# Optimization experiments

Hardware: AMD Instinct MI355X
Metric: run time of the kernel (lower is better)

## Reference

```python
import jax, jax.numpy as jnp
import numpy as np

EPS = 1e-5

def bn(x, gamma, beta, axes):
    # Training-mode batch norm: normalize over batch(+spatial) axes, channel-last layout.
    m = x.mean(axes, keepdims=True)
    v = x.var(axes, keepdims=True)
    return gamma * (x - m) * jax.lax.rsqrt(v + EPS) + beta

def spa_group(k, xyz, feat):
    # PCT-style grouping: k-NN in xyz space, concat(neighbor-center, center).
    # xyz: (B,N,3)  feat: (B,N,C)  ->  (B,N,k,2C)
    sq = jnp.sum(xyz * xyz, axis=-1)  # (B,N)
    d = sq[:, :, None] + sq[:, None, :] - 2.0 * jnp.einsum('bnd,bmd->bnm', xyz, xyz)
    _, idx = jax.lax.top_k(-d, k)  # (B,N,k) nearest-neighbor indices (includes self)
    grouped = jax.vmap(lambda f, i: f[i])(feat, idx)  # (B,N,k,C) irregular gather
    center = feat[:, :, None, :]
    return jnp.concatenate([grouped - center, jnp.broadcast_to(center, grouped.shape)], axis=-1)

def local_op(x, w1, g1, b1, w2, g2, b2):
    # x: (B,N,K,Ci) -> conv1x1/BN/ReLU x2 over the K window, then max-pool over K -> (B,N,Co)
    h = jnp.einsum('bnkc,oc->bnko', x, w1)
    h = jax.nn.relu(bn(h, g1, b1, (0, 1, 2)))
    h = jnp.einsum('bnkc,oc->bnko', h, w2)
    h = jax.nn.relu(bn(h, g2, b2, (0, 1, 2)))
    return h.max(axis=2)

def setup_inputs():
    key = jax.random.key(0)
    ks = jax.random.split(key, 7)
    B, N = 4, 2048
    d_i, d_h1, d_h2, d_h3, d_o = 3, 64, 256, 512, 1024
    def w(k_, o, i):
        return jax.random.normal(k_, (o, i), jnp.float32) * (1.0 / np.sqrt(i))
    return {
        'xyz': jax.random.normal(ks[0], (B, N, d_i), jnp.float32),
        'w_c1': w(ks[1], d_h1, d_i), 'g_c1': jnp.ones((d_h1,), jnp.float32), 'b_c1': jnp.zeros((d_h1,), jnp.float32),
        'w_c2': w(ks[2], d_h2, d_h1), 'g_c2': jnp.ones((d_h2,), jnp.float32), 'b_c2': jnp.zeros((d_h2,), jnp.float32),
        'w_l0a': w(ks[3], d_h3, d_h3), 'g_l0a': jnp.ones((d_h3,), jnp.float32), 'b_l0a': jnp.zeros((d_h3,), jnp.float32),
        'w_l0b': w(ks[4], d_h3, d_h3), 'g_l0b': jnp.ones((d_h3,), jnp.float32), 'b_l0b': jnp.zeros((d_h3,), jnp.float32),
        'w_l1a': w(ks[5], d_o, d_o), 'g_l1a': jnp.ones((d_o,), jnp.float32), 'b_l1a': jnp.zeros((d_o,), jnp.float32),
        'w_l1b': w(ks[6], d_o, d_o), 'g_l1b': jnp.ones((d_o,), jnp.float32), 'b_l1b': jnp.zeros((d_o,), jnp.float32),
        'k': 8,
    }

def reference(xyz, w_c1, g_c1, b_c1, w_c2, g_c2, b_c2,
              w_l0a, g_l0a, b_l0a, w_l0b, g_l0b, b_l0b,
              w_l1a, g_l1a, b_l1a, w_l1b, g_l1b, b_l1b, k):
    # Stem: conv1x1-BN-ReLU x2 in (B,N,C) layout (equivalent to torch (B,C,N) with BN over (0,2))
    h = jax.nn.relu(bn(jnp.einsum('bnc,oc->bno', xyz, w_c1), g_c1, b_c1, (0, 1)))
    h = jax.nn.relu(bn(jnp.einsum('bnc,oc->bno', h, w_c2), g_c2, b_c2, (0, 1)))
    g = spa_group(k, xyz, h)                                   # (B,N,k,512)
    h = local_op(g, w_l0a, g_l0a, b_l0a, w_l0b, g_l0b, b_l0b)  # (B,N,512)
    g = spa_group(k, xyz, h)                                   # (B,N,k,1024)
    h = local_op(g, w_l1a, g_l1a, b_l1a, w_l1b, g_l1b, b_l1b)  # (B,N,1024)
    return jnp.transpose(h, (0, 2, 1))  # (B, d_o, N) to match torch output layout
```

## Files before the change

### kernel.cpp

```cpp
#include <hip/hip_runtime.h>

typedef unsigned short u16;
typedef __attribute__((ext_vector_type(8))) short s16x8;
typedef __attribute__((ext_vector_type(8))) __bf16 bf16x8;
typedef __attribute__((ext_vector_type(8))) unsigned short u16x8;
typedef __attribute__((ext_vector_type(4))) float f32x4;

#define BN_EPS 1e-5f

__device__ u16   g_Z[(size_t)65536 * 1024];
__device__ u16   g_F[(size_t)8192 * 2048];
__device__ float g_pooled[(size_t)8192 * 1024];
__device__ float g_h2pre[8192 * 256];
__device__ u16   g_h2b[8192 * 256];
__device__ u16   g_hl0b[8192 * 512];
__device__ float g_y1[8192 * 64];
__device__ u16   g_wm0a[1024 * 256];
__device__ u16   g_w0b[512 * 512];
__device__ u16   g_wm1a[2048 * 512];
__device__ u16   g_w1b[1024 * 1024];
__device__ int   g_nidx[65536];
__device__ float g_st[24 * 1024];

#define S(i) (g_st + (i) * 1024)

static __device__ __forceinline__ float bf2f(u16 u) {
  unsigned int x = ((unsigned int)u) << 16;
  return __builtin_bit_cast(float, x);
}
static __device__ __forceinline__ u16 f2bf(float f) {
  unsigned int x = __builtin_bit_cast(unsigned int, f);
  x += 0x7fffu + ((x >> 16) & 1u);
  return (u16)(x >> 16);
}
static __device__ __forceinline__ f32x4 mfma16x16(s16x8 a, s16x8 b, f32x4 c) {
  return __builtin_amdgcn_mfma_f32_16x16x32_bf16(
      __builtin_bit_cast(bf16x8, a), __builtin_bit_cast(bf16x8, b), c, 0, 0, 0);
}
static __device__ __forceinline__ void gl_lds16(const void* g, void* l) {
  __builtin_amdgcn_global_load_lds((const __attribute__((address_space(1))) void*)g,
                                   (__attribute__((address_space(3))) void*)l, 16, 0, 0);
}

__global__ void k_zero() {
  int i = blockIdx.x * 256 + threadIdx.x;
  if (i < 12 * 1024) g_st[i] = 0.f;
}

__global__ void k_lin1(const float* __restrict__ xyz, const float* __restrict__ w) {
  __shared__ float ls[64], lq[64];
  int t = threadIdx.x;
  if (t < 64) { ls[t] = 0.f; lq[t] = 0.f; }
  __syncthreads();
  int e = blockIdx.x * 256 + t;
  int row = e >> 6, ch = e & 63;
  float x0 = xyz[row * 3], x1 = xyz[row * 3 + 1], x2 = xyz[row * 3 + 2];
  float v = x0 * w[ch * 3] + x1 * w[ch * 3 + 1] + x2 * w[ch * 3 + 2];
  g_y1[e] = v;
  atomicAdd(&ls[ch], v);
  atomicAdd(&lq[ch], v * v);
  __syncthreads();
  if (t < 64) { atomicAdd(&S(0)[t], ls[t]); atomicAdd(&S(1)[t], lq[t]); }
}

__global__ void k_stats(const float* __restrict__ g, const float* __restrict__ b,
                        int si_s, int si_q, int si_sc, int si_bi, float invcnt) {
  int c = blockIdx.x * 64 + threadIdx.x;
  float m = S(si_s)[c] * invcnt;
  float v = S(si_q)[c] * invcnt - m * m;
  float sc = g[c] * rsqrtf(v + BN_EPS);
  S(si_sc)[c] = sc;
  S(si_bi)[c] = b[c] - m * sc;
}

__global__ void k_lin2(const float* __restrict__ w) {
  __shared__ float hrow[64];
  int t = threadIdx.x;
  float wr[64];
#pragma unroll
  for (int i = 0; i < 64; i++) wr[i] = w[t * 64 + i];
  const float* sc1 = S(12);
  const float* bi1 = S(13);
  float ps = 0.f, pq = 0.f;
  int r0 = blockIdx.x * 16;
  for (int r = 0; r < 16; r++) {
    if (t < 64) {
      float v = g_y1[(r0 + r) * 64 + t];
      v = v * sc1[t] + bi1[t];
      hrow[t] = v > 0.f ? v : 0.f;
    }
    __syncthreads();
    float acc = 0.f;
#pragma unroll
    for (int i = 0; i < 64; i++) acc += hrow[i] * wr[i];
    g_h2pre[(r0 + r) * 256 + t] = acc;
    ps += acc;
    pq += acc * acc;
    __syncthreads();
  }
  atomicAdd(&S(2)[t], ps);
  atomicAdd(&S(3)[t], pq);
}

__global__ void k_bnrelu_h2() {
  int i = blockIdx.x * 256 + threadIdx.x;
  if (i >= 8192 * 256) return;
  int c = i & 255;
  float v = g_h2pre[i] * S(14)[c] + S(15)[c];
  g_h2b[i] = f2bf(v > 0.f ? v : 0.f);
}

__global__ __launch_bounds__(256) void k_knn(const float* __restrict__ xyz) {
  int t = threadIdx.x, lane = t & 63, w = t >> 6;
  int qn = blockIdx.x * 4 + w;
  int b = qn >> 11;
  const float* xb = xyz + (size_t)b * 2048 * 3;
  int ql = qn & 2047;
  float qx = xb[ql * 3], qy = xb[ql * 3 + 1], qz = xb[ql * 3 + 2];
  float qsq = qx * qx + qy * qy + qz * qz;

  float bd[8];
  int bi[8];
#pragma unroll
  for (int i = 0; i < 8; i++) { bd[i] = 1e30f; bi[i] = 0x7fffffff; }

#pragma unroll 4
  for (int i = 0; i < 32; i++) {
    int j = lane + i * 64;
    float x = xb[j * 3], y = xb[j * 3 + 1], z = xb[j * 3 + 2];
    float sq = x * x + y * y + z * z;
    float d = qsq + sq - 2.0f * (qx * x + qy * y + qz * z);
    if (d < bd[7]) {
      bd[7] = d; bi[7] = j;
#pragma unroll
      for (int p = 7; p > 0; p--) {
        if (bd[p] < bd[p - 1]) {
          float td = bd[p]; bd[p] = bd[p - 1]; bd[p - 1] = td;
          int ti = bi[p]; bi[p] = bi[p - 1]; bi[p - 1] = ti;
        }
      }
    }
  }

  int keep = 0;
#pragma unroll
  for (int r = 0; r < 8; r++) {
    float md = bd[0];
    int mi = bi[0];
#pragma unroll
    for (int s = 1; s < 64; s <<= 1) {
      float od = __shfl_xor(md, s, 64);
      int oi = __shfl_xor(mi, s, 64);
      if (od < md || (od == md && oi < mi)) { md = od; mi = oi; }
    }
    bool own = (bd[0] == md) && (bi[0] == mi);
    if (own) {
#pragma unroll
      for (int p = 0; p < 7; p++) { bd[p] = bd[p + 1]; bi[p] = bi[p + 1]; }
      bd[7] = 1e30f; bi[7] = 0x7fffffff;
    }
    if (lane == r) keep = mi;
  }
  if (lane < 8) g_nidx[qn * 8 + lane] = b * 2048 + keep;
}

__global__ void k_prep_w(const float* __restrict__ src, int which, int n) {
  int i = blockIdx.x * 256 + threadIdx.x;
  if (i >= n) return;
  u16* dst = which == 1 ? g_w0b : g_w1b;
  dst[i] = f2bf(src[i]);
}

__global__ void k_prep_wst(const float* __restrict__ src, int which, int lc, int N, int n) {
  int i = blockIdx.x * 256 + threadIdx.x;
  if (i >= n) return;
  int C = 1 << lc;
  int r = i >> lc, c = i & (C - 1);
  float v;
  if (r < N) v = src[r * 2 * C + c];
  else { int o = r - N; v = src[o * 2 * C + C + c] - src[o * 2 * C + c]; }
  u16* dst = which == 0 ? g_wm0a : g_wm1a;
  dst[i] = f2bf(v);
}


#define GEMM_PRO()                                                     \
  int t = threadIdx.x, lane = t & 63, w = t >> 6;                      \
  int chunk = gridDim.x >> 3;                                          \
  int idx = ((int)blockIdx.x & 7) * chunk + ((int)blockIdx.x >> 3);    \
  int bx = idx & ((1 << lbx) - 1), by = idx >> lbx;                    \
  int wm = w >> 2, wn = w & 3;                                         \
  int l15 = lane & 15, lq = lane >> 4;                                 \
  int gcs = (((lane & 3) ^ ((lane >> 3) & 3))) * 8;                    \
  int rA0 = w * 16 + (lane >> 2), rA1 = rA0 + 128;                     \
  int ldsA0 = w * 512, ldsA1 = 4096 + w * 512;                         \
  int ksw = (lq ^ ((l15 >> 1) & 3)) * 8;                               \
  f32x4 acc[8][4];                                                     \
  _Pragma("unroll") for (int m = 0; m < 8; m++)                        \
  _Pragma("unroll") for (int n = 0; n < 4; n++)                        \
      acc[m][n] = f32x4{0.f, 0.f, 0.f, 0.f};

#define GEMM_LOOP(STG)                                                   \
  STG(0, 0) STG(1, 1) STG(2, 2)                                          \
  asm volatile("s_waitcnt vmcnt(8)" ::: "memory");                       \
  __builtin_amdgcn_s_barrier();                                          \
  asm volatile("" ::: "memory");                                         \
  for (int ks = 0; ks < nk; ks++) {                                      \
    int b = ks & 3;                                                      \
    int kst = (ks + 3 < nk) ? ks + 3 : nk - 1;                           \
    STG(kst, (ks + 3) & 3)                                               \
    s16x8 af[8], bf[4];                                                  \
    _Pragma("unroll") for (int m = 0; m < 8; m++)                        \
        af[m] = *(const s16x8*)&As[b][(wm * 128 + m * 16 + l15) * 32 + ksw]; \
    _Pragma("unroll") for (int n = 0; n < 4; n++)                        \
        bf[n] = *(const s16x8*)&Bs[b][(wn * 64 + n * 16 + l15) * 32 + ksw];  \
    __builtin_amdgcn_s_setprio(1);                                       \
    _Pragma("unroll") for (int m = 0; m < 8; m++)                        \
    _Pragma("unroll") for (int n = 0; n < 4; n++)                        \
        acc[m][n] = mfma16x16(af[m], bf[n], acc[m][n]);                  \
    __builtin_amdgcn_s_setprio(0);                                       \
    asm volatile("s_waitcnt vmcnt(8)" ::: "memory");                     \
    __builtin_amdgcn_s_barrier();                                        \
    asm volatile("" ::: "memory");                                       \
  }

#define GEMM_STATS(si_s, si_q)                                           \
  if (t < 256) { cs[t] = 0.f; cq[t] = 0.f; }                             \
  __syncthreads();                                                       \
  _Pragma("unroll") for (int n = 0; n < 4; n++) {                        \
    float ssum = 0.f, ssq = 0.f;                                         \
    _Pragma("unroll") for (int m = 0; m < 8; m++)                        \
    _Pragma("unroll") for (int j = 0; j < 4; j++) {                      \
      float v = acc[m][n][j];                                            \
      ssum += v;                                                         \
      ssq += v * v;                                                      \
    }                                                                    \
    int col = wn * 64 + n * 16 + l15;                                    \
    atomicAdd(&cs[col], ssum);                                           \
    atomicAdd(&cq[col], ssq);                                            \
  }                                                                      \
  __syncthreads();                                                       \
  if (t < 256) {                                                         \
    atomicAdd(&S(si_s)[bx * 256 + t], cs[t]);                            \
    atomicAdd(&S(si_q)[bx * 256 + t], cq[t]);                            \
  }

__global__ __launch_bounds__(512) void k_fgemm(int layer, int C, int N2, int lbx) {
  __shared__ u16 As[4][8192];
  __shared__ u16 Bs[4][8192];
  const u16* feat = layer == 0 ? g_h2b : g_hl0b;
  const u16* W = layer == 0 ? g_wm0a : g_wm1a;
  GEMM_PRO();
  int nk = C >> 5;
  const u16* srA0 = feat + (size_t)(by * 256 + rA0) * C + gcs;
  const u16* srA1 = feat + (size_t)(by * 256 + rA1) * C + gcs;
  const u16* srB0 = W + (size_t)(bx * 256 + rA0) * C + gcs;
  const u16* srB1 = W + (size_t)(bx * 256 + rA1) * C + gcs;

#define STG_F(KT, BUF)                                                        \
  {                                                                           \
    int kg_ = (KT) * 32;                                                      \
    gl_lds16(srA0 + kg_, &As[BUF][ldsA0]);                                    \
    gl_lds16(srA1 + kg_, &As[BUF][ldsA1]);                                    \
    gl_lds16(srB0 + kg_, &Bs[BUF][ldsA0]);                                    \
    gl_lds16(srB1 + kg_, &Bs[BUF][ldsA1]);                                    \
  }

  GEMM_LOOP(STG_F)
#undef STG_F

#pragma unroll
  for (int m = 0; m < 8; m++) {
    int rbase = by * 256 + wm * 128 + m * 16 + lq * 4;
#pragma unroll
    for (int n = 0; n < 4; n++) {
      int col = bx * 256 + wn * 64 + n * 16 + l15;
#pragma unroll
      for (int j = 0; j < 4; j++)
        g_F[(size_t)(rbase + j) * N2 + col] = f2bf(acc[m][n][j]);
    }
  }
}

__global__ __launch_bounds__(512) void k_combine(int N, int lgc, int si_s, int si_q) {
  __shared__ float Ls[1024], Lq[1024];
  int t = threadIdx.x;
  int chs8 = 1 << lgc;
  int c8 = t & (chs8 - 1);
  int g = t >> lgc;
  int G = 512 >> lgc;
  int rpg = 256 / G;
  int row0 = blockIdx.x * 256 + g * rpg;
  int ch0 = c8 * 8;
  int N2 = 2 * N;
  float ss[8], sq[8];
#pragma unroll
  for (int j = 0; j < 8; j++) { ss[j] = 0.f; sq[j] = 0.f; }

  for (int r = row0; r < row0 + rpg; r++) {
    int nb = g_nidx[r];
    int ct = r >> 3;
    u16x8 a = *(const u16x8*)(g_F + (size_t)nb * N2 + ch0);
    u16x8 b = *(const u16x8*)(g_F + (size_t)ct * N2 + N + ch0);
    u16x8 o;
#pragma unroll
    for (int j = 0; j < 8; j++) {
      float z = bf2f(a[j]) + bf2f(b[j]);
      o[j] = f2bf(z);
      ss[j] += z;
      sq[j] += z * z;
    }
    *(u16x8*)(g_Z + (size_t)r * N + ch0) = o;
  }

  for (int c = t; c < N; c += 512) { Ls[c] = 0.f; Lq[c] = 0.f; }
  __syncthreads();
#pragma unroll
  for (int j = 0; j < 8; j++) {
    atomicAdd(&Ls[ch0 + j], ss[j]);
    atomicAdd(&Lq[ch0 + j], sq[j]);
  }
  __syncthreads();
  for (int c = t; c < N; c += 512) {
    atomicAdd(&S(si_s)[c], Ls[c]);
    atomicAdd(&S(si_q)[c], Lq[c]);
  }
}

__global__ __launch_bounds__(512) void k_gp8(int layer, int K, int N, int si_s,
                                             int si_q, int lbx) {
  __shared__ u16 As[4][8192];
  __shared__ u16 Bs[4][8192];
  __shared__ float cs[256], cq[256];
  const u16* W = layer == 0 ? g_w0b : g_w1b;
  GEMM_PRO();
  int nk = K >> 5;
  const u16* srA0 = g_Z + (size_t)(by * 256 + rA0) * K + gcs;
  const u16* srA1 = g_Z + (size_t)(by * 256 + rA1) * K + gcs;
  const u16* srB0 = W + (size_t)(bx * 256 + rA0) * K + gcs;
  const u16* srB1 = W + (size_t)(bx * 256 + rA1) * K + gcs;

#define STG_P(KT, BUF)                                                        \
  {                                                                           \
    int kg_ = (KT) * 32;                                                      \
    gl_lds16(srA0 + kg_, &As[BUF][ldsA0]);                                    \
    gl_lds16(srA1 + kg_, &As[BUF][ldsA1]);                                    \
    gl_lds16(srB0 + kg_, &Bs[BUF][ldsA0]);                                    \
    gl_lds16(srB1 + kg_, &Bs[BUF][ldsA1]);                                    \
  }

  GEMM_LOOP(STG_P)
#undef STG_P

#pragma unroll
  for (int m = 0; m < 8; m++) {
    int prow = by * 32 + wm * 16 + m * 2 + (lq >> 1);
#pragma unroll
    for (int n = 0; n < 4; n++) {
      float v4 = fmaxf(fmaxf(acc[m][n][0], acc[m][n][1]), fmaxf(acc[m][n][2], acc[m][n][3]));
      float v8 = fmaxf(v4, __shfl_xor(v4, 16, 64));
      if ((lane & 16) == 0) {
        int col = bx * 256 + wn * 64 + n * 16 + l15;
        g_pooled[(size_t)prow * N + col] = v8;
      }
    }
  }
  GEMM_STATS(si_s, si_q)
}

__global__ void k_bnrelu_z(int si_sc, int si_bi, int cmask, size_t n8) {
  size_t i = (size_t)blockIdx.x * 256 + threadIdx.x;
  size_t stride = (size_t)gridDim.x * 256;
  const float* sc = S(si_sc);
  const float* bi = S(si_bi);
  for (; i < n8; i += stride) {
    u16x8 v = *(const u16x8*)(g_Z + i * 8);
    int c0 = (int)((i * 8) & (size_t)cmask);
    u16x8 o;
#pragma unroll
    for (int j = 0; j < 8; j++) {
      float f = bf2f(v[j]) * sc[c0 + j] + bi[c0 + j];
      o[j] = f2bf(f > 0.f ? f : 0.f);
    }
    *(u16x8*)(g_Z + i * 8) = o;
  }
}

__global__ void k_bnrelu_pool() {
  int i = blockIdx.x * 256 + threadIdx.x;
  if (i >= 8192 * 512) return;
  int c = i & 511;
  float v = g_pooled[i] * S(18)[c] + S(19)[c];
  g_hl0b[i] = f2bf(v > 0.f ? v : 0.f);
}

__global__ void k_final_t(float* __restrict__ out) {
  __shared__ float tile[64][65];
  int b = blockIdx.z;
  int nb = blockIdx.y;
  int cb = blockIdx.x;
  int t = threadIdx.x;
  int cl = t & 63;
  int c = cb * 64 + cl;
  float sc = S(22)[c], bi = S(23)[c];
  for (int nl = t >> 6; nl < 64; nl += 4) {
    float v = g_pooled[(size_t)(b * 2048 + nb * 64 + nl) * 1024 + c] * sc + bi;
    tile[nl][cl] = v > 0.f ? v : 0.f;
  }
  __syncthreads();
  int nl2 = t & 63;
  for (int ci = t >> 6; ci < 64; ci += 4) {
    out[((size_t)b * 1024 + cb * 64 + ci) * 2048 + nb * 64 + nl2] = tile[nl2][ci];
  }
}

extern "C" void kernel_launch(void* const* d_in, const int* in_sizes, int n_in,
                              void* d_out, int out_size, void* d_ws, size_t ws_size,
                              hipStream_t stream) {
  const float* xyz  = (const float*)d_in[0];
  const float* w_c1 = (const float*)d_in[1];
  const float* g_c1 = (const float*)d_in[2];
  const float* b_c1 = (const float*)d_in[3];
  const float* w_c2 = (const float*)d_in[4];
  const float* g_c2 = (const float*)d_in[5];
  const float* b_c2 = (const float*)d_in[6];
  const float* w_l0a = (const float*)d_in[7];
  const float* g_l0a = (const float*)d_in[8];
  const float* b_l0a = (const float*)d_in[9];
  const float* w_l0b = (const float*)d_in[10];
  const float* g_l0b = (const float*)d_in[11];
  const float* b_l0b = (const float*)d_in[12];
  const float* w_l1a = (const float*)d_in[13];
  const float* g_l1a = (const float*)d_in[14];
  const float* b_l1a = (const float*)d_in[15];
  const float* w_l1b = (const float*)d_in[16];
  const float* g_l1b = (const float*)d_in[17];
  const float* b_l1b = (const float*)d_in[18];
  float* out = (float*)d_out;

  k_zero<<<48, 256, 0, stream>>>();

  k_lin1<<<2048, 256, 0, stream>>>(xyz, w_c1);
  k_stats<<<1, 64, 0, stream>>>(g_c1, b_c1, 0, 1, 12, 13, 1.f / 8192.f);
  k_lin2<<<512, 256, 0, stream>>>(w_c2);
  k_stats<<<4, 64, 0, stream>>>(g_c2, b_c2, 2, 3, 14, 15, 1.f / 8192.f);
  k_bnrelu_h2<<<8192, 256, 0, stream>>>();

  k_knn<<<2048, 256, 0, stream>>>(xyz);

  k_prep_wst<<<1024, 256, 0, stream>>>(w_l0a, 0, 8, 512, 262144);
  k_prep_w<<<1024, 256, 0, stream>>>(w_l0b, 1, 262144);
  k_prep_wst<<<4096, 256, 0, stream>>>(w_l1a, 2, 9, 1024, 1048576);
  k_prep_w<<<4096, 256, 0, stream>>>(w_l1b, 3, 1048576);

  k_fgemm<<<128, 512, 0, stream>>>(0, 256, 1024, 2);
  k_combine<<<256, 512, 0, stream>>>(512, 6, 4, 5);
  k_stats<<<8, 64, 0, stream>>>(g_l0a, b_l0a, 4, 5, 16, 17, 1.f / 65536.f);
  k_bnrelu_z<<<2048, 256, 0, stream>>>(16, 17, 511, (size_t)65536 * 512 / 8);
  k_gp8<<<512, 512, 0, stream>>>(0, 512, 512, 6, 7, 1);
  k_stats<<<8, 64, 0, stream>>>(g_l0b, b_l0b, 6, 7, 18, 19, 1.f / 65536.f);
  k_bnrelu_pool<<<16384, 256, 0, stream>>>();

  k_fgemm<<<256, 512, 0, stream>>>(1, 512, 2048, 3);
  k_combine<<<256, 512, 0, stream>>>(1024, 7, 8, 9);
  k_stats<<<16, 64, 0, stream>>>(g_l1a, b_l1a, 8, 9, 20, 21, 1.f / 65536.f);
  k_bnrelu_z<<<2048, 256, 0, stream>>>(20, 21, 1023, (size_t)65536 * 1024 / 8);
  k_gp8<<<1024, 512, 0, stream>>>(1, 1024, 1024, 10, 11, 2);
  k_stats<<<16, 64, 0, stream>>>(g_l1b, b_l1b, 10, 11, 22, 23, 1.f / 65536.f);
  k_final_t<<<dim3(16, 32, 4), 256, 0, stream>>>(out);
}
```

Measured before the change: 773.4 us.

## Restructure GEMM mainloop into 8-wave ping-pong with BK=64 double buffering

Replaces the 4-stage BK=32 LDS ring in both GEMM kernels with a double-buffered BK=64 tile and a new XOR swizzle. Each k-tile is split into four quadrant MFMA phases, with barriers between them, and the global-to-LDS loads for tile k+2 are interleaved between phases. The goal is to overlap LDS reads, global prefetch and MFMA work more finely and to cut per-k-step barrier overhead. The cost is more barriers per tile, tighter vmcnt bookkeeping, and only two buffers of prefetch depth.

```diff
diff --git a/kernel.cpp b/kernel.cpp
--- a/kernel.cpp
+++ b/kernel.cpp
@@ -184,44 +184,118 @@
 }
 
 
-#define GEMM_PRO()                                                     \
-  int t = threadIdx.x, lane = t & 63, w = t >> 6;                      \
-  int chunk = gridDim.x >> 3;                                          \
-  int idx = ((int)blockIdx.x & 7) * chunk + ((int)blockIdx.x >> 3);    \
-  int bx = idx & ((1 << lbx) - 1), by = idx >> lbx;                    \
-  int wm = w >> 2, wn = w & 3;                                         \
-  int l15 = lane & 15, lq = lane >> 4;                                 \
-  int gcs = (((lane & 3) ^ ((lane >> 3) & 3))) * 8;                    \
-  int rA0 = w * 16 + (lane >> 2), rA1 = rA0 + 128;                     \
-  int ldsA0 = w * 512, ldsA1 = 4096 + w * 512;                         \
-  int ksw = (lq ^ ((l15 >> 1) & 3)) * 8;                               \
-  f32x4 acc[8][4];                                                     \
-  _Pragma("unroll") for (int m = 0; m < 8; m++)                        \
-  _Pragma("unroll") for (int n = 0; n < 4; n++)                        \
+#define BARRIER_F() { __builtin_amdgcn_s_barrier(); asm volatile("" ::: "memory"); }
+
+#define GEMM8_PRO()                                                       \
+  int t = threadIdx.x, lane = t & 63, w = t >> 6;                         \
+  int chunk = gridDim.x >> 3;                                             \
+  int idx = ((int)blockIdx.x & 7) * chunk + ((int)blockIdx.x >> 3);       \
+  int bx = idx & ((1 << lbx) - 1), by = idx >> lbx;                       \
+  int wm = w >> 2, wn = w & 3;                                            \
+  int l15 = lane & 15, lq = lane >> 4;                                    \
+  int c0 = lq ^ (l15 & 7);                                                \
+  int ab0 = wm * 8192 + l15 * 64 + c0 * 8;                                \
+  int ab1 = wm * 8192 + l15 * 64 + (c0 ^ 4) * 8;                          \
+  int bb0 = (wn >> 1) * 8192 + (wn & 1) * 4096 + l15 * 64 + c0 * 8;       \
+  int bb1 = (wn >> 1) * 8192 + (wn & 1) * 4096 + l15 * 64 + (c0 ^ 4) * 8; \
+  int sr = t >> 3, skc = (t & 7) ^ ((t >> 3) & 7);                        \
+  f32x4 acc[8][4];                                                        \
+  _Pragma("unroll") for (int m = 0; m < 8; m++)                           \
+  _Pragma("unroll") for (int n = 0; n < 4; n++)                           \
       acc[m][n] = f32x4{0.f, 0.f, 0.f, 0.f};
 
-#define GEMM_LOOP(STG)                                                   \
-  STG(0, 0) STG(1, 1) STG(2, 2)                                          \
-  asm volatile("s_waitcnt vmcnt(8)" ::: "memory");                       \
-  __builtin_amdgcn_s_barrier();                                          \
-  asm volatile("" ::: "memory");                                         \
-  for (int ks = 0; ks < nk; ks++) {                                      \
-    int b = ks & 3;                                                      \
-    int kst = (ks + 3 < nk) ? ks + 3 : nk - 1;                           \
-    STG(kst, (ks + 3) & 3)                                               \
-    s16x8 af[8], bf[4];                                                  \
-    _Pragma("unroll") for (int m = 0; m < 8; m++)                        \
-        af[m] = *(const s16x8*)&As[b][(wm * 128 + m * 16 + l15) * 32 + ksw]; \
-    _Pragma("unroll") for (int n = 0; n < 4; n++)                        \
-        bf[n] = *(const s16x8*)&Bs[b][(wn * 64 + n * 16 + l15) * 32 + ksw];  \
-    __builtin_amdgcn_s_setprio(1);                                       \
-    _Pragma("unroll") for (int m = 0; m < 8; m++)                        \
-    _Pragma("unroll") for (int n = 0; n < 4; n++)                        \
-        acc[m][n] = mfma16x16(af[m], bf[n], acc[m][n]);                  \
-    __builtin_amdgcn_s_setprio(0);                                       \
-    asm volatile("s_waitcnt vmcnt(8)" ::: "memory");                     \
-    __builtin_amdgcn_s_barrier();                                        \
-    asm volatile("" ::: "memory");                                       \
+#define GEMM8_LOOP(Ag, Bg)                                                    \
+  const u16* a0 = (Ag) + (size_t)(by * 256 + sr) * K + skc * 8;               \
+  const u16* b0 = (Bg) + (size_t)(bx * 256 + sr) * K + skc * 8;               \
+  _Pragma("unroll") for (int tl = 0; tl < 2; tl++) {                          \
+    u16* AW = As + tl * 16384; u16* BW = Bs + tl * 16384;                     \
+    int cc = tl * 64;                                                         \
+    gl_lds16(a0 + cc, AW + t * 8);                                            \
+    gl_lds16(a0 + (size_t)128 * K + cc, AW + 8192 + t * 8);                   \
+    gl_lds16(a0 + (size_t)64 * K + cc, AW + 4096 + t * 8);                    \
+    gl_lds16(a0 + (size_t)192 * K + cc, AW + 12288 + t * 8);                  \
+    gl_lds16(b0 + cc, BW + t * 8);                                            \
+    gl_lds16(b0 + (size_t)64 * K + cc, BW + 4096 + t * 8);                    \
+    gl_lds16(b0 + (size_t)128 * K + cc, BW + 8192 + t * 8);                   \
+    gl_lds16(b0 + (size_t)192 * K + cc, BW + 12288 + t * 8);                  \
+  }                                                                           \
+  asm volatile("s_waitcnt vmcnt(8)" ::: "memory");                            \
+  BARRIER_F();                                                                \
+  for (int kt = 0; kt < nk; kt++) {                                           \
+    u16* AsR = As + (kt & 1) * 16384;                                         \
+    u16* BsR = Bs + (kt & 1) * 16384;                                         \
+    bool st = (kt + 2 < nk);                                                  \
+    int c2 = (kt + 2) * 64;                                                   \
+    s16x8 af[8], bfl[4], bfh[4];                                              \
+                                       \
+    _Pragma("unroll") for (int ks = 0; ks < 2; ks++)                          \
+    _Pragma("unroll") for (int m = 0; m < 4; m++)                             \
+        af[ks * 4 + m] = *(const s16x8*)&AsR[(ks ? ab1 : ab0) + m * 1024];    \
+    _Pragma("unroll") for (int ks = 0; ks < 2; ks++)                          \
+    _Pragma("unroll") for (int n = 0; n < 2; n++)                             \
+        bfl[ks * 2 + n] = *(const s16x8*)&BsR[(ks ? bb1 : bb0) + n * 1024];   \
+    BARRIER_F();                                                              \
+    asm volatile("s_waitcnt lgkmcnt(0)" ::: "memory");                        \
+    __builtin_amdgcn_sched_barrier(0);                                        \
+    __builtin_amdgcn_s_setprio(1);                                            \
+    _Pragma("unroll") for (int ks = 0; ks < 2; ks++)                          \
+    _Pragma("unroll") for (int m = 0; m < 4; m++)                             \
+    _Pragma("unroll") for (int n = 0; n < 2; n++)                             \
+        acc[m][n] = mfma16x16(af[ks * 4 + m], bfl[ks * 2 + n], acc[m][n]);    \
+    __builtin_amdgcn_s_setprio(0);                                            \
+    BARRIER_F();                                                              \
+       \
+    if (st) {                                                                 \
+      gl_lds16(a0 + c2, AsR + t * 8);                                         \
+      gl_lds16(a0 + (size_t)128 * K + c2, AsR + 8192 + t * 8);                \
+    }                                                                         \
+    _Pragma("unroll") for (int ks = 0; ks < 2; ks++)                          \
+    _Pragma("unroll") for (int n = 0; n < 2; n++)                             \
+        bfh[ks * 2 + n] = *(const s16x8*)&BsR[(ks ? bb1 : bb0) + 2048 + n * 1024]; \
+    BARRIER_F();                                                              \
+    asm volatile("s_waitcnt lgkmcnt(0)" ::: "memory");                        \
+    __builtin_amdgcn_sched_barrier(0);                                        \
+    __builtin_amdgcn_s_setprio(1);                                            \
+    _Pragma("unroll") for (int ks = 0; ks < 2; ks++)                          \
+    _Pragma("unroll") for (int m = 0; m < 4; m++)                             \
+    _Pragma("unroll") for (int n = 0; n < 2; n++)                             \
+        acc[m][2 + n] = mfma16x16(af[ks * 4 + m], bfh[ks * 2 + n], acc[m][2 + n]); \
+    __builtin_amdgcn_s_setprio(0);                                            \
+    BARRIER_F();                                                              \
+                      \
+    if (st) {                                                                 \
+      gl_lds16(b0 + c2, BsR + t * 8);                                         \
+      gl_lds16(b0 + (size_t)64 * K + c2, BsR + 4096 + t * 8);                 \
+      gl_lds16(b0 + (size_t)128 * K + c2, BsR + 8192 + t * 8);                \
+      gl_lds16(b0 + (size_t)192 * K + c2, BsR + 12288 + t * 8);               \
+    }                                                                         \
+    _Pragma("unroll") for (int ks = 0; ks < 2; ks++)                          \
+    _Pragma("unroll") for (int m = 0; m < 4; m++)                             \
+        af[ks * 4 + m] = *(const s16x8*)&AsR[(ks ? ab1 : ab0) + 4096 + m * 1024]; \
+    BARRIER_F();                                                              \
+    asm volatile("s_waitcnt lgkmcnt(0)" ::: "memory");                        \
+    __builtin_amdgcn_sched_barrier(0);                                        \
+    __builtin_amdgcn_s_setprio(1);                                            \
+    _Pragma("unroll") for (int ks = 0; ks < 2; ks++)                          \
+    _Pragma("unroll") for (int m = 0; m < 4; m++)                             \
+    _Pragma("unroll") for (int n = 0; n < 2; n++)                             \
+        acc[4 + m][n] = mfma16x16(af[ks * 4 + m], bfl[ks * 2 + n], acc[4 + m][n]); \
+    __builtin_amdgcn_s_setprio(0);                                            \
+    BARRIER_F();                                                              \
+      \
+    if (st) {                                                                 \
+      gl_lds16(a0 + (size_t)64 * K + c2, AsR + 4096 + t * 8);                 \
+      gl_lds16(a0 + (size_t)192 * K + c2, AsR + 12288 + t * 8);               \
+    }                                                                         \
+    __builtin_amdgcn_s_setprio(1);                                            \
+    _Pragma("unroll") for (int ks = 0; ks < 2; ks++)                          \
+    _Pragma("unroll") for (int m = 0; m < 4; m++)                             \
+    _Pragma("unroll") for (int n = 0; n < 2; n++)                             \
+        acc[4 + m][2 + n] = mfma16x16(af[ks * 4 + m], bfh[ks * 2 + n], acc[4 + m][2 + n]); \
+    __builtin_amdgcn_s_setprio(0);                                            \
+    if (kt < nk - 2) { asm volatile("s_waitcnt vmcnt(6)" ::: "memory"); }     \
+    else             { asm volatile("s_waitcnt vmcnt(0)" ::: "memory"); }     \
+    BARRIER_F();                                                              \
   }
 
 #define GEMM_STATS(si_s, si_q)                                           \
@@ -246,28 +320,13 @@
   }
 
 __global__ __launch_bounds__(512) void k_fgemm(int layer, int C, int N2, int lbx) {
-  __shared__ u16 As[4][8192];
-  __shared__ u16 Bs[4][8192];
+  __shared__ u16 As[2 * 16384];
+  __shared__ u16 Bs[2 * 16384];
   const u16* feat = layer == 0 ? g_h2b : g_hl0b;
   const u16* W = layer == 0 ? g_wm0a : g_wm1a;
-  GEMM_PRO();
-  int nk = C >> 5;
-  const u16* srA0 = feat + (size_t)(by * 256 + rA0) * C + gcs;
-  const u16* srA1 = feat + (size_t)(by * 256 + rA1) * C + gcs;
-  const u16* srB0 = W + (size_t)(bx * 256 + rA0) * C + gcs;
-  const u16* srB1 = W + (size_t)(bx * 256 + rA1) * C + gcs;
-
-#define STG_F(KT, BUF)                                                        \
-  {                                                                           \
-    int kg_ = (KT) * 32;                                                      \
-    gl_lds16(srA0 + kg_, &As[BUF][ldsA0]);                                    \
-    gl_lds16(srA1 + kg_, &As[BUF][ldsA1]);                                    \
-    gl_lds16(srB0 + kg_, &Bs[BUF][ldsA0]);                                    \
-    gl_lds16(srB1 + kg_, &Bs[BUF][ldsA1]);                                    \
-  }
-
-  GEMM_LOOP(STG_F)
-#undef STG_F
+  int K = C, nk = C >> 6;
+  GEMM8_PRO();
+  GEMM8_LOOP(feat, W)
 
 #pragma unroll
   for (int m = 0; m < 8; m++) {
@@ -327,30 +386,15 @@
   }
 }
 
-__global__ __launch_bounds__(512) void k_gp8(int layer, int K, int N, int si_s,
+__global__ __launch_bounds__(512) void k_gp8(int layer, int Kp, int N, int si_s,
                                              int si_q, int lbx) {
-  __shared__ u16 As[4][8192];
-  __shared__ u16 Bs[4][8192];
+  __shared__ u16 As[2 * 16384];
+  __shared__ u16 Bs[2 * 16384];
   __shared__ float cs[256], cq[256];
   const u16* W = layer == 0 ? g_w0b : g_w1b;
-  GEMM_PRO();
-  int nk = K >> 5;
-  const u16* srA0 = g_Z + (size_t)(by * 256 + rA0) * K + gcs;
-  const u16* srA1 = g_Z + (size_t)(by * 256 + rA1) * K + gcs;
-  const u16* srB0 = W + (size_t)(bx * 256 + rA0) * K + gcs;
-  const u16* srB1 = W + (size_t)(bx * 256 + rA1) * K + gcs;
-
-#define STG_P(KT, BUF)                                                        \
-  {                                                                           \
-    int kg_ = (KT) * 32;                                                      \
-    gl_lds16(srA0 + kg_, &As[BUF][ldsA0]);                                    \
-    gl_lds16(srA1 + kg_, &As[BUF][ldsA1]);                                    \
-    gl_lds16(srB0 + kg_, &Bs[BUF][ldsA0]);                                    \
-    gl_lds16(srB1 + kg_, &Bs[BUF][ldsA1]);                                    \
-  }
-
-  GEMM_LOOP(STG_P)
-#undef STG_P
+  int K = Kp, nk = Kp >> 6;
+  GEMM8_PRO();
+  GEMM8_LOOP(g_Z, W)
 
 #pragma unroll
   for (int m = 0; m < 8; m++) {
```

Measured after the change: 737.4 us. -4.7%, faster.
